# Kernel optimization log

Measured on AMD Instinct MI355X. Metric: run time of the kernel, lower is better.

## Reference

```python
import jax, jax.numpy as jnp
import numpy as np

NJ = 12
# shift buffer: inverse of the fixed 12x12 permutation matrix (= its transpose)
_idx = np.array([0, 1, 6, 2, 3, 8, 9, 7, 4, 5, 10, 11])
_P = np.zeros((NJ, NJ), np.float32)
_P[np.arange(NJ), _idx] = 1.0
SHIFT = jnp.asarray(_P.T)


def _bn(x, g, b, eps=1e-5):
    # BatchNorm2d in training mode: biased var over (batch, positions) per channel
    m = x.mean(axis=(0, 1), keepdims=True)
    v = x.var(axis=(0, 1), keepdims=True)
    return (x - m) * jax.lax.rsqrt(v + eps) * g + b


def setup_inputs() -> dict:
    key = jax.random.key(0)
    ks = jax.random.split(key, 10)
    B, D, E = 16384, 128, 128
    Din = D + E
    f32 = jnp.float32
    inp = {
        "gout": jax.random.normal(ks[0], (B, NJ, D), f32),
        "eout": jax.random.normal(ks[1], (B, NJ, E), f32),
        "ev_shift": jax.random.uniform(ks[2], (NJ, NJ), f32),
        "ve_shift": jax.random.uniform(ks[3], (NJ, NJ), f32),
        "W_ev": jax.random.normal(ks[4], (D, Din), f32) * 0.001,
        "W_ve": jax.random.normal(ks[5], (D, Din), f32) * 0.001,
        "W1": jax.random.normal(ks[6], (D, 3 * D), f32) * 0.001,
        "W2": jax.random.normal(ks[7], (D, 3 * D), f32) * 0.001,
        "W3": jax.random.normal(ks[8], (D, 2 * D), f32) * 0.001,
        "W4": jax.random.normal(ks[9], (D, 3 * D), f32) * 0.001,
    }
    for name in ["ev", "ve", "1", "2", "3", "4"]:
        inp["g_" + name] = jnp.ones((D,), f32)
        inp["b_" + name] = jnp.zeros((D,), f32)
    return inp


def reference(gout, eout, ev_shift, ve_shift, W_ev, g_ev, b_ev, W_ve, g_ve, b_ve,
              W1, g_1, b_1, W2, g_2, b_2, W3, g_3, b_3, W4, g_4, b_4):
    # gout: [B, 12, D], eout: [B, 12, E]
    ev_g = jnp.einsum('ij,bjd->bid', ev_shift, gout)
    ve_g = jnp.einsum('ij,bjd->bid', ve_shift, gout)
    # conv1x1 over channel dim == linear over feature dim; BN stats over (B, joints)
    ef = jax.nn.relu(_bn(jnp.einsum('bnc,dc->bnd', jnp.concatenate([eout, ev_g], -1), W_ev), g_ev, b_ev))
    vf = jax.nn.relu(_bn(jnp.einsum('bnc,dc->bnd', jnp.concatenate([ve_g, eout], -1), W_ve), g_ve, b_ve))
    # node_res blocks: per-group gather+concat -> linear -> BN (stats over B*group_positions)
    op1 = _bn(jnp.concatenate([ef[:, 0], ef[:, 1], ef[:, 5]], -1)[:, None] @ W1.T, g_1, b_1)
    op2_in = jnp.stack([
        jnp.concatenate([vf[:, 0], ef[:, 3], ef[:, 7]], -1),
        jnp.concatenate([vf[:, 5], ef[:, 7], ef[:, 8]], -1)], axis=1)
    op2 = _bn(op2_in @ W2.T, g_2, b_2)
    op3_in = jnp.stack([
        jnp.concatenate([vf[:, 1], ef[:, 2]], -1),
        jnp.concatenate([vf[:, 3], ef[:, 4]], -1),
        jnp.concatenate([vf[:, 8], ef[:, 9]], -1),
        jnp.concatenate([vf[:, 10], ef[:, 11]], -1)], axis=1)
    op3 = _bn(op3_in @ W3.T, g_3, b_3)
    op4 = _bn(jnp.concatenate([vf[:, 6], vf[:, 7], ef[:, 10]], -1)[:, None] @ W4.T, g_4, b_4)
    op5 = jnp.stack([vf[:, 2], vf[:, 4], vf[:, 9], vf[:, 11]], axis=1)
    res = jnp.concatenate([op1, op2, op3, op4, op5], axis=1)  # [B, 12, D]
    res = jnp.einsum('ij,bjd->bid', SHIFT, res)
    return jax.nn.relu(gout + res)
```

## Files before the change

### kernel.cpp

```cpp
#include <hip/hip_runtime.h>
#include <hip/hip_bf16.h>

#define BTOT 16384
typedef unsigned short u16;
typedef __attribute__((ext_vector_type(8))) short bf16x8;
typedef __attribute__((ext_vector_type(8))) unsigned short u16x8;
typedef __attribute__((ext_vector_type(4))) float f32x4;

#define MFMA16(a, b, c) __builtin_amdgcn_mfma_f32_16x16x32_bf16(a, b, c, 0, 0, 0)
#define NSLOT 16

__device__ __forceinline__ u16 f2b(float f) {
  unsigned int i = __float_as_uint(f);
  return (u16)((i + 0x7FFFu + ((i >> 16) & 1u)) >> 16);
}
__device__ __forceinline__ float b2f(u16 u) {
  return __uint_as_float(((unsigned int)u) << 16);
}
__device__ __forceinline__ unsigned pk2(float x, float y) {
  __hip_bfloat162 h = __float22bfloat162_rn(make_float2(x, y));
  unsigned r; __builtin_memcpy(&r, &h, 4); return r;
}
__device__ __forceinline__ bf16x8 pack8(float4 lo, float4 hi) {
  union { unsigned u[4]; bf16x8 v; } r;
  r.u[0] = pk2(lo.x, lo.y); r.u[1] = pk2(lo.z, lo.w);
  r.u[2] = pk2(hi.x, hi.y); r.u[3] = pk2(hi.z, hi.w);
  return r.v;
}
__device__ __forceinline__ void glds16(const void* g, void* l) {
  __builtin_amdgcn_global_load_lds(
      (const __attribute__((address_space(1))) void*)g,
      (__attribute__((address_space(3))) void*)l, 16, 0, 0);
}

__device__ const int c_mb[8][3]  = {{0,0,0},{1,0,0},{1,0,0},{1,0,0},{1,0,0},{1,0,0},{1,0,0},{1,1,0}};
__device__ const int c_mj[8][3]  = {{0,1,5},{0,3,7},{5,7,8},{1,2,0},{3,4,0},{8,9,0},{10,11,0},{6,7,10}};
__device__ const int c_opof[8]   = {0,1,1,2,2,2,2,3};
__device__ const int c_jmap[12]  = {0,1,3,4,8,9,2,7,5,6,10,11};
__device__ const int c_vj[4]     = {2,4,9,11};

__global__ __launch_bounds__(256) void k_prep(
    const float* __restrict__ wev, const float* __restrict__ wve,
    const float* __restrict__ w1, const float* __restrict__ w2,
    const float* __restrict__ w3, const float* __restrict__ w4,
    u16* __restrict__ wb, float* __restrict__ stats)
{
  int id = blockIdx.x * 256 + threadIdx.x;
  if (blockIdx.x == 0) {
    for (int i = threadIdx.x; i < NSLOT * 1536; i += 256) stats[i] = 0.f;
  }
  const float* src; int base, K, local;
  if (id < 32768)       { src = wev; base = 0;      K = 256; local = id; }
  else if (id < 65536)  { src = wve; base = 32768;  K = 256; local = id - 32768; }
  else if (id < 114688) { src = w1;  base = 65536;  K = 384; local = id - 65536; }
  else if (id < 163840) { src = w2;  base = 114688; K = 384; local = id - 114688; }
  else if (id < 196608) { src = w3;  base = 163840; K = 256; local = id - 163840; }
  else if (id < 245760) { src = w4;  base = 196608; K = 384; local = id - 245760 + 49152; }
  else return;
  if (id >= 196608 && id < 245760) local = id - 196608;
  int d = local / K, k = local - d * K;
  int dk = (base == 32768) ? (k ^ 128) : k;
  int dest = base + (dk >> 6) * 8192 + d * 64 + ((dk & 63) ^ ((d & 7) << 3));
  wb[dest] = f2b(src[local]);
}

__global__ __launch_bounds__(256, 2) void k_stage1(
    const float* __restrict__ gout, const float* __restrict__ eout,
    const float* __restrict__ evs, const float* __restrict__ ves,
    const u16* __restrict__ wb_ev, const u16* __restrict__ wb_ve,
    u16* __restrict__ y_ev, u16* __restrict__ y_ve, float* __restrict__ stats)
{
  __shared__ __align__(16) char lds[81920];
  char* se = lds;
  char* sm = lds + 24576;
  char* sw = lds + 49152;
  float* s_red = (float*)(lds + 49152);

  const int tid = threadIdx.x;
  const int l = tid & 63, wv = tid >> 6;
  const int wm = wv >> 1, wn = wv & 1;
  const int b0 = blockIdx.x * 8;
  const int kq = (l >> 4) * 8;
  const int bb = tid >> 5;
  const int d4 = (tid & 31) * 4;

  auto wstage = [&](const u16* wmat, int c, char* buf) {
    char* wvb = buf + wv * 1024;
    #pragma unroll
    for (int q = 0; q < 4; ++q)
      glds16(&wmat[c * 8192 + tid * 8 + q * 2048], wvb + q * 4096);
  };

  wstage(wb_ev, 0, sw);

  {
    float mev[12][4];
    #pragma unroll
    for (int n = 0; n < 12; ++n)
      #pragma unroll
      for (int q = 0; q < 4; ++q) mev[n][q] = 0.f;
    #pragma unroll
    for (int j = 0; j < 12; ++j) {
      float4 g4 = *(const float4*)&gout[((size_t)(b0 + bb) * 12 + j) * 128 + d4];
      float4 e4 = *(const float4*)&eout[((size_t)(b0 + bb) * 12 + j) * 128 + d4];
      int row = bb * 12 + j;
      uint2 ep = make_uint2(pk2(e4.x, e4.y), pk2(e4.z, e4.w));
      *(uint2*)(se + row * 256 + ((d4 * 2) ^ ((row & 7) << 4))) = ep;
      #pragma unroll
      for (int n = 0; n < 12; ++n) {
        float w = evs[n * 12 + j];
        mev[n][0] = fmaf(w, g4.x, mev[n][0]); mev[n][1] = fmaf(w, g4.y, mev[n][1]);
        mev[n][2] = fmaf(w, g4.z, mev[n][2]); mev[n][3] = fmaf(w, g4.w, mev[n][3]);
      }
    }
    #pragma unroll
    for (int n = 0; n < 12; ++n) {
      int row = bb * 12 + n;
      uint2 mp = make_uint2(pk2(mev[n][0], mev[n][1]), pk2(mev[n][2], mev[n][3]));
      *(uint2*)(sm + row * 256 + ((d4 * 2) ^ ((row & 7) << 4))) = mp;
    }
  }

  float sE[4] = {0,0,0,0}, qE[4] = {0,0,0,0}, sV[4] = {0,0,0,0}, qV[4] = {0,0,0,0};

  auto run_pass = [&](const u16* wmat, const u16* nextw, u16* yout, char* dump,
                      float* sS, float* qS) {
    f32x4 acc[3][4];
    #pragma unroll
    for (int mi = 0; mi < 3; ++mi)
      #pragma unroll
      for (int ni = 0; ni < 4; ++ni) acc[mi][ni] = (f32x4){0.f, 0.f, 0.f, 0.f};

    for (int c = 0; c < 4; ++c) {
      __syncthreads();
      if (c < 3) wstage(wmat, c + 1, sw + (((c + 1) & 1) ? 16384 : 0));
      else if (nextw) wstage(nextw, 0, sw);
      const char* xb = (c < 2) ? se : sm;
      const char* swb = sw + ((c & 1) ? 16384 : 0);
      #pragma unroll
      for (int kt = 0; kt < 2; ++kt) {
        bf16x8 a[3], bq[4];
        const int kb = (((c & 1) * 64 + kt * 32 + kq)) * 2;
        #pragma unroll
        for (int mi = 0; mi < 3; ++mi) {
          int row = (wm * 3 + mi) * 16 + (l & 15);
          a[mi] = *(const bf16x8*)(xb + row * 256 + (kb ^ ((row & 7) << 4)));
        }
        const int kw = (kt * 32 + kq) * 2;
        #pragma unroll
        for (int ni = 0; ni < 4; ++ni) {
          int n = (wn * 4 + ni) * 16 + (l & 15);
          bq[ni] = *(const bf16x8*)(swb + n * 128 + (kw ^ ((n & 7) << 4)));
        }
        #pragma unroll
        for (int mi = 0; mi < 3; ++mi)
          #pragma unroll
          for (int ni = 0; ni < 4; ++ni)
            acc[mi][ni] = MFMA16(a[mi], bq[ni], acc[mi][ni]);
      }
    }
    __syncthreads();
    #pragma unroll
    for (int mi = 0; mi < 3; ++mi)
      #pragma unroll
      for (int ni = 0; ni < 4; ++ni)
        #pragma unroll
        for (int q = 0; q < 4; ++q) {
          float v = acc[mi][ni][q];
          sS[ni] += v; qS[ni] += v * v;
          int row = (wm * 3 + mi) * 16 + (l >> 4) * 4 + q;
          int cb = ((wn * 4 + ni) * 16 + (l & 15)) * 2;
          *(u16*)(dump + row * 256 + (cb ^ ((row & 7) << 4))) = f2b(v);
        }
    __syncthreads();
    #pragma unroll
    for (int q = 0; q < 6; ++q) {
      int i = tid + q * 256;
      int row = i >> 4, cb = (i & 15) * 16;
      u16x8 v = *(const u16x8*)(dump + row * 256 + (cb ^ ((row & 7) << 4)));
      *(u16x8*)&yout[(size_t)(b0 * 12 + row) * 128 + (i & 15) * 8] = v;
    }
    __syncthreads();
  };

  run_pass(wb_ev, wb_ve, y_ev, sm, sE, qE);

  {
    float mve[12][4];
    #pragma unroll
    for (int n = 0; n < 12; ++n)
      #pragma unroll
      for (int q = 0; q < 4; ++q) mve[n][q] = 0.f;
    #pragma unroll
    for (int j = 0; j < 12; ++j) {
      float4 g4 = *(const float4*)&gout[((size_t)(b0 + bb) * 12 + j) * 128 + d4];
      #pragma unroll
      for (int n = 0; n < 12; ++n) {
        float w = ves[n * 12 + j];
        mve[n][0] = fmaf(w, g4.x, mve[n][0]); mve[n][1] = fmaf(w, g4.y, mve[n][1]);
        mve[n][2] = fmaf(w, g4.z, mve[n][2]); mve[n][3] = fmaf(w, g4.w, mve[n][3]);
      }
    }
    #pragma unroll
    for (int n = 0; n < 12; ++n) {
      int row = bb * 12 + n;
      uint2 mp = make_uint2(pk2(mve[n][0], mve[n][1]), pk2(mve[n][2], mve[n][3]));
      *(uint2*)(sm + row * 256 + ((d4 * 2) ^ ((row & 7) << 4))) = mp;
    }
  }

  run_pass(wb_ve, (const u16*)nullptr, y_ve, se, sV, qV);

  s_red[tid] = 0.f; s_red[tid + 256] = 0.f;
  __syncthreads();
  #pragma unroll
  for (int ni = 0; ni < 4; ++ni) {
    float a1 = sE[ni], b1 = qE[ni], a2 = sV[ni], b2 = qV[ni];
    a1 += __shfl_xor(a1, 16); a1 += __shfl_xor(a1, 32);
    b1 += __shfl_xor(b1, 16); b1 += __shfl_xor(b1, 32);
    a2 += __shfl_xor(a2, 16); a2 += __shfl_xor(a2, 32);
    b2 += __shfl_xor(b2, 16); b2 += __shfl_xor(b2, 32);
    if (l < 16) {
      int ch = (wn * 4 + ni) * 16 + l;
      atomicAdd(&s_red[ch], a1);       atomicAdd(&s_red[128 + ch], b1);
      atomicAdd(&s_red[256 + ch], a2); atomicAdd(&s_red[384 + ch], b2);
    }
  }
  __syncthreads();
  const int sb = (blockIdx.x & (NSLOT - 1)) * 1536;
  atomicAdd(&stats[sb + tid], s_red[tid]);
  atomicAdd(&stats[sb + 256 + tid], s_red[256 + tid]);
}

__global__ void k_fin1(const float* __restrict__ stats, float* __restrict__ scale,
                       const float* __restrict__ gev, const float* __restrict__ bev,
                       const float* __restrict__ gve, const float* __restrict__ bve)
{
  int t = threadIdx.x;
  int m = t >> 7, d = t & 127;
  float s = 0.f, q = 0.f;
  #pragma unroll
  for (int sl = 0; sl < NSLOT; ++sl) {
    s += stats[sl * 1536 + m * 256 + d];
    q += stats[sl * 1536 + m * 256 + 128 + d];
  }
  float cnt = (float)(BTOT * 12);
  float mean = s / cnt, var = q / cnt - mean * mean;
  float rs = rsqrtf(var + 1e-5f);
  float g = m ? gve[d] : gev[d];
  float b = m ? bve[d] : bev[d];
  float a = g * rs;
  scale[m * 256 + d] = a;
  scale[m * 256 + 128 + d] = b - mean * a;
}

__global__ __launch_bounds__(256, 4) void k_stage2(
    const u16* __restrict__ y_ev, const u16* __restrict__ y_ve,
    const float* __restrict__ scale,
    const u16* __restrict__ wb1, const u16* __restrict__ wb2,
    const u16* __restrict__ wb3, const u16* __restrict__ wb4,
    u16* __restrict__ y_op, float* __restrict__ stats)
{
  __shared__ __align__(16) u16 s_w[128 * 64];
  __shared__ __align__(16) u16 s_d[32 * 128];
  __shared__ float s_scale[512];
  __shared__ float s_red[256];
  char* sw = (char*)s_w; char* sd = (char*)s_d;

  const int tid = threadIdx.x, l = tid & 63, wv = tid >> 6;
  const int mw = wv & 1, nw = wv >> 1;
  const int r = blockIdx.x & 7;
  const int b0 = (blockIdx.x >> 3) * 32;
  const int Kr = (r >= 3 && r <= 6) ? 256 : 384;
  const u16* wr = (r == 0) ? wb1 : (r <= 2) ? wb2 : (r <= 6) ? wb3 : wb4;
  const int o = c_opof[r];
  const int j0 = c_mj[r][0], j1 = c_mj[r][1], j2 = c_mj[r][2];
  const int m0 = c_mb[r][0], m1 = c_mb[r][1], m2 = c_mb[r][2];

  for (int i = tid; i < 512; i += 256) s_scale[i] = scale[i];
  s_red[tid] = 0.f;

  f32x4 acc[4];
  #pragma unroll
  for (int ni = 0; ni < 4; ++ni) acc[ni] = (f32x4){0.f, 0.f, 0.f, 0.f};

  const int nch = Kr >> 6;
  const int kq = (l >> 4) * 8;
  const int batch = b0 + mw * 16 + (l & 15);

  for (int c = 0; c < nch; ++c) {
    {
      char* wvb = sw + wv * 1024;
      #pragma unroll
      for (int q = 0; q < 4; ++q)
        glds16(&wr[c * 8192 + tid * 8 + q * 2048], wvb + q * 4096);
    }
    __syncthreads();
    const int s = c >> 1;
    const int j = (s == 0) ? j0 : (s == 1) ? j1 : j2;
    const int mb = (s == 0) ? m0 : (s == 1) ? m1 : m2;
    const int sb = mb ? 256 : 0;
    const u16* ys = mb ? y_ve : y_ev;
    #pragma unroll
    for (int kt = 0; kt < 2; ++kt) {
      const int chan = (c & 1) * 64 + kt * 32 + kq;
      u16x8 u = *(const u16x8*)&ys[((size_t)batch * 12 + j) * 128 + chan];
      float4 a0 = *(const float4*)&s_scale[sb + chan];
      float4 a1 = *(const float4*)&s_scale[sb + chan + 4];
      float4 c0 = *(const float4*)&s_scale[sb + 128 + chan];
      float4 c1 = *(const float4*)&s_scale[sb + 128 + chan + 4];
      float4 lo, hi;
      lo.x = fmaxf(fmaf(b2f(u[0]), a0.x, c0.x), 0.f);
      lo.y = fmaxf(fmaf(b2f(u[1]), a0.y, c0.y), 0.f);
      lo.z = fmaxf(fmaf(b2f(u[2]), a0.z, c0.z), 0.f);
      lo.w = fmaxf(fmaf(b2f(u[3]), a0.w, c0.w), 0.f);
      hi.x = fmaxf(fmaf(b2f(u[4]), a1.x, c1.x), 0.f);
      hi.y = fmaxf(fmaf(b2f(u[5]), a1.y, c1.y), 0.f);
      hi.z = fmaxf(fmaf(b2f(u[6]), a1.z, c1.z), 0.f);
      hi.w = fmaxf(fmaf(b2f(u[7]), a1.w, c1.w), 0.f);
      bf16x8 afrag = pack8(lo, hi);
      const int kw = (kt * 32 + kq) * 2;
      #pragma unroll
      for (int ni = 0; ni < 4; ++ni) {
        int n = (nw * 4 + ni) * 16 + (l & 15);
        bf16x8 b = *(const bf16x8*)(sw + n * 128 + (kw ^ ((n & 7) << 4)));
        acc[ni] = MFMA16(afrag, b, acc[ni]);
      }
    }
    __syncthreads();
  }

  #pragma unroll
  for (int ni = 0; ni < 4; ++ni) {
    float s1 = 0.f, q1 = 0.f;
    #pragma unroll
    for (int q = 0; q < 4; ++q) {
      float v = acc[ni][q];
      s1 += v; q1 += v * v;
      int row = mw * 16 + (l >> 4) * 4 + q;
      int cb = ((nw * 4 + ni) * 16 + (l & 15)) * 2;
      *(u16*)(sd + row * 256 + (cb ^ ((row & 7) << 4))) = f2b(v);
    }
    s1 += __shfl_xor(s1, 16); s1 += __shfl_xor(s1, 32);
    q1 += __shfl_xor(q1, 16); q1 += __shfl_xor(q1, 32);
    if (l < 16) {
      int ch = (nw * 4 + ni) * 16 + l;
      atomicAdd(&s_red[ch], s1);
      atomicAdd(&s_red[128 + ch], q1);
    }
  }
  __syncthreads();
  #pragma unroll
  for (int q = 0; q < 2; ++q) {
    int i = tid + q * 256;
    int row = i >> 4, cb = (i & 15) * 16;
    u16x8 v = *(const u16x8*)(sd + row * 256 + (cb ^ ((row & 7) << 4)));
    *(u16x8*)&y_op[((size_t)(b0 + row) * 8 + r) * 128 + (i & 15) * 8] = v;
  }
  const int sb2 = (blockIdx.x & (NSLOT - 1)) * 1536;
  atomicAdd(&stats[sb2 + 512 + o * 256 + tid], s_red[tid]);
}

__global__ void k_fin2(const float* __restrict__ stats, float* __restrict__ scale,
    const float* __restrict__ g1, const float* __restrict__ b1,
    const float* __restrict__ g2, const float* __restrict__ b2,
    const float* __restrict__ g3, const float* __restrict__ b3,
    const float* __restrict__ g4, const float* __restrict__ b4)
{
  int t = threadIdx.x;
  int o = t >> 7, d = t & 127;
  float s = 0.f, q = 0.f;
  #pragma unroll
  for (int sl = 0; sl < NSLOT; ++sl) {
    s += stats[sl * 1536 + 512 + o * 256 + d];
    q += stats[sl * 1536 + 512 + o * 256 + 128 + d];
  }
  float cnt = (o == 0 || o == 3) ? 16384.f : (o == 1 ? 32768.f : 65536.f);
  float mean = s / cnt, var = q / cnt - mean * mean;
  float rs = rsqrtf(var + 1e-5f);
  const float* gp = (o == 0) ? g1 : (o == 1) ? g2 : (o == 2) ? g3 : g4;
  const float* bp = (o == 0) ? b1 : (o == 1) ? b2 : (o == 2) ? b3 : b4;
  float a = gp[d] * rs;
  scale[512 + o * 256 + d] = a;
  scale[512 + o * 256 + 128 + d] = bp[d] - mean * a;
}

__global__ __launch_bounds__(256) void k_stage3(
    const u16* __restrict__ y_op, const u16* __restrict__ y_ve,
    const float* __restrict__ scale, const float* __restrict__ gout,
    float* __restrict__ out)
{
  const int stride = gridDim.x * 256;
  const int total = BTOT * 12 * 32;
  for (int id = blockIdx.x * 256 + threadIdx.x; id < total; id += stride) {
    int b = id / 384;
    int rem = id - b * 384;
    int i = rem >> 5;
    int d4 = (rem & 31) * 4;
    int j = c_jmap[i];
    float4 v;
    if (j < 8) {
      ushort4 u = *(const ushort4*)&y_op[((size_t)b * 8 + j) * 128 + d4];
      int o = c_opof[j];
      float4 a4 = *(const float4*)&scale[512 + o * 256 + d4];
      float4 c4 = *(const float4*)&scale[512 + o * 256 + 128 + d4];
      v.x = fmaf(b2f(u.x), a4.x, c4.x);
      v.y = fmaf(b2f(u.y), a4.y, c4.y);
      v.z = fmaf(b2f(u.z), a4.z, c4.z);
      v.w = fmaf(b2f(u.w), a4.w, c4.w);
    } else {
      int jv = c_vj[j - 8];
      ushort4 u = *(const ushort4*)&y_ve[((size_t)b * 12 + jv) * 128 + d4];
      float4 a4 = *(const float4*)&scale[256 + d4];
      float4 c4 = *(const float4*)&scale[384 + d4];
      v.x = fmaxf(fmaf(b2f(u.x), a4.x, c4.x), 0.f);
      v.y = fmaxf(fmaf(b2f(u.y), a4.y, c4.y), 0.f);
      v.z = fmaxf(fmaf(b2f(u.z), a4.z, c4.z), 0.f);
      v.w = fmaxf(fmaf(b2f(u.w), a4.w, c4.w), 0.f);
    }
    float4 g4 = *(const float4*)&gout[((size_t)b * 12 + i) * 128 + d4];
    float4 r4;
    r4.x = fmaxf(g4.x + v.x, 0.f);
    r4.y = fmaxf(g4.y + v.y, 0.f);
    r4.z = fmaxf(g4.z + v.z, 0.f);
    r4.w = fmaxf(g4.w + v.w, 0.f);
    *(float4*)&out[((size_t)b * 12 + i) * 128 + d4] = r4;
  }
}

extern "C" void kernel_launch(void* const* d_in, const int* in_sizes, int n_in,
                              void* d_out, int out_size, void* d_ws, size_t ws_size,
                              hipStream_t stream) {
  (void)in_sizes; (void)n_in; (void)out_size; (void)ws_size;
  const float* gout = (const float*)d_in[0];
  const float* eout = (const float*)d_in[1];
  const float* evs  = (const float*)d_in[2];
  const float* ves  = (const float*)d_in[3];
  const float* wev  = (const float*)d_in[4];
  const float* wve  = (const float*)d_in[5];
  const float* w1   = (const float*)d_in[6];
  const float* w2   = (const float*)d_in[7];
  const float* w3   = (const float*)d_in[8];
  const float* w4   = (const float*)d_in[9];
  const float* g_ev = (const float*)d_in[10]; const float* b_ev = (const float*)d_in[11];
  const float* g_ve = (const float*)d_in[12]; const float* b_ve = (const float*)d_in[13];
  const float* g_1  = (const float*)d_in[14]; const float* b_1  = (const float*)d_in[15];
  const float* g_2  = (const float*)d_in[16]; const float* b_2  = (const float*)d_in[17];
  const float* g_3  = (const float*)d_in[18]; const float* b_3  = (const float*)d_in[19];
  const float* g_4  = (const float*)d_in[20]; const float* b_4  = (const float*)d_in[21];

  char* ws = (char*)d_ws;
  u16*   y_ev  = (u16*)ws;
  u16*   y_ve  = (u16*)(ws + 50331648);
  u16*   y_op  = (u16*)(ws + 100663296);
  u16*   wb    = (u16*)(ws + 134217728);
  float* stats = (float*)(ws + 134709248);
  float* scale = (float*)(ws + 134807552);

  k_prep<<<960, 256, 0, stream>>>(wev, wve, w1, w2, w3, w4, wb, stats);
  k_stage1<<<2048, 256, 0, stream>>>(gout, eout, evs, ves, wb, wb + 32768, y_ev, y_ve, stats);
  k_fin1<<<1, 256, 0, stream>>>(stats, scale, g_ev, b_ev, g_ve, b_ve);
  k_stage2<<<4096, 256, 0, stream>>>(y_ev, y_ve, scale, wb + 65536, wb + 114688, wb + 163840, wb + 196608, y_op, stats);
  k_fin2<<<1, 512, 0, stream>>>(stats, scale, g_1, b_1, g_2, b_2, g_3, b_3, g_4, b_4);
  k_stage3<<<4096, 256, 0, stream>>>(y_op, y_ve, scale, gout, (float*)d_out);
}
```

Measured before the change: 207.8 us.

## Hold eout MFMA fragments in registers and halve weight staging to raise occupancy

Stage 1 no longer stages eout through LDS. Each wave loads its eout A-fragments straight from global into registers and packs them to bf16. The weight staging buffer is split into half-chunks of 32 K-columns with a new 64-byte-row swizzle, and the prep kernel lays out the ev/ve weights to match. Shared memory drops from 80 KB to about 42 KB and launch bounds rise to 3 blocks per CU, aiming for more occupancy. In exchange there are more barriers per pass and more registers held for eout fragments, which could cause spills under the tighter register budget.

Result: slower. 308.8 us (+48.6%).

```diff
diff --git a/kernel.cpp b/kernel.cpp
--- a/kernel.cpp
+++ b/kernel.cpp
@@ -55,26 +55,27 @@
   else if (id < 114688) { src = w1;  base = 65536;  K = 384; local = id - 65536; }
   else if (id < 163840) { src = w2;  base = 114688; K = 384; local = id - 114688; }
   else if (id < 196608) { src = w3;  base = 163840; K = 256; local = id - 163840; }
-  else if (id < 245760) { src = w4;  base = 196608; K = 384; local = id - 245760 + 49152; }
+  else if (id < 245760) { src = w4;  base = 196608; K = 384; local = id - 196608; }
   else return;
-  if (id >= 196608 && id < 245760) local = id - 196608;
   int d = local / K, k = local - d * K;
-  int dk = (base == 32768) ? (k ^ 128) : k;
-  int dest = base + (dk >> 6) * 8192 + d * 64 + ((dk & 63) ^ ((d & 7) << 3));
-  wb[dest] = f2b(src[local]);
-}
-
-__global__ __launch_bounds__(256, 2) void k_stage1(
+  if (base < 65536) {
+    int dk = (base == 32768) ? (k ^ 128) : k;
+    int c = dk >> 6, kt = (dk >> 5) & 1, kk = dk & 31;
+    wb[base + c * 8192 + kt * 4096 + d * 32 + (kk ^ ((d & 3) << 3))] = f2b(src[local]);
+  } else {
+    wb[base + (k >> 6) * 8192 + d * 64 + ((k & 63) ^ ((d & 7) << 3))] = f2b(src[local]);
+  }
+}
+
+__global__ __launch_bounds__(256, 3) void k_stage1(
     const float* __restrict__ gout, const float* __restrict__ eout,
     const float* __restrict__ evs, const float* __restrict__ ves,
     const u16* __restrict__ wb_ev, const u16* __restrict__ wb_ve,
     u16* __restrict__ y_ev, u16* __restrict__ y_ve, float* __restrict__ stats)
 {
-  __shared__ __align__(16) char lds[81920];
-  char* se = lds;
-  char* sm = lds + 24576;
-  char* sw = lds + 49152;
-  float* s_red = (float*)(lds + 49152);
+  __shared__ __align__(16) char sm[24576];
+  __shared__ __align__(16) char sw[16384];
+  __shared__ float s_red[512];
 
   const int tid = threadIdx.x;
   const int l = tid & 63, wv = tid >> 6;
@@ -84,11 +85,12 @@
   const int bb = tid >> 5;
   const int d4 = (tid & 31) * 4;
 
-  auto wstage = [&](const u16* wmat, int c, char* buf) {
+  auto wstage = [&](const u16* wmat, int p, char* buf) {
+    const u16* pb = wmat + (p >> 1) * 8192 + (p & 1) * 4096;
     char* wvb = buf + wv * 1024;
     #pragma unroll
-    for (int q = 0; q < 4; ++q)
-      glds16(&wmat[c * 8192 + tid * 8 + q * 2048], wvb + q * 4096);
+    for (int q = 0; q < 2; ++q)
+      glds16(&pb[tid * 8 + q * 2048], wvb + q * 4096);
   };
 
   wstage(wb_ev, 0, sw);
@@ -102,10 +104,6 @@
     #pragma unroll
     for (int j = 0; j < 12; ++j) {
       float4 g4 = *(const float4*)&gout[((size_t)(b0 + bb) * 12 + j) * 128 + d4];
-      float4 e4 = *(const float4*)&eout[((size_t)(b0 + bb) * 12 + j) * 128 + d4];
-      int row = bb * 12 + j;
-      uint2 ep = make_uint2(pk2(e4.x, e4.y), pk2(e4.z, e4.w));
-      *(uint2*)(se + row * 256 + ((d4 * 2) ^ ((row & 7) << 4))) = ep;
       #pragma unroll
       for (int n = 0; n < 12; ++n) {
         float w = evs[n * 12 + j];
@@ -121,9 +119,23 @@
     }
   }
 
+  bf16x8 ea[2][2][3];
+  #pragma unroll
+  for (int c2 = 0; c2 < 2; ++c2)
+    #pragma unroll
+    for (int kt = 0; kt < 2; ++kt)
+      #pragma unroll
+      for (int mi = 0; mi < 3; ++mi) {
+        int row = wm * 48 + mi * 16 + (l & 15);
+        const float* p = eout + ((size_t)(b0 * 12) + row) * 128 + c2 * 64 + kt * 32 + kq;
+        float4 u0 = *(const float4*)p;
+        float4 u1 = *(const float4*)(p + 4);
+        ea[c2][kt][mi] = pack8(u0, u1);
+      }
+
   float sE[4] = {0,0,0,0}, qE[4] = {0,0,0,0}, sV[4] = {0,0,0,0}, qV[4] = {0,0,0,0};
 
-  auto run_pass = [&](const u16* wmat, const u16* nextw, u16* yout, char* dump,
+  auto run_pass = [&](const u16* wmat, const u16* nextw, u16* yout,
                       float* sS, float* qS) {
     f32x4 acc[3][4];
     #pragma unroll
@@ -131,33 +143,35 @@
       #pragma unroll
       for (int ni = 0; ni < 4; ++ni) acc[mi][ni] = (f32x4){0.f, 0.f, 0.f, 0.f};
 
-    for (int c = 0; c < 4; ++c) {
+    #pragma unroll
+    for (int p = 0; p < 8; ++p) {
       __syncthreads();
-      if (c < 3) wstage(wmat, c + 1, sw + (((c + 1) & 1) ? 16384 : 0));
+      if (p < 7) wstage(wmat, p + 1, sw + (((p + 1) & 1) ? 8192 : 0));
       else if (nextw) wstage(nextw, 0, sw);
-      const char* xb = (c < 2) ? se : sm;
-      const char* swb = sw + ((c & 1) ? 16384 : 0);
-      #pragma unroll
-      for (int kt = 0; kt < 2; ++kt) {
-        bf16x8 a[3], bq[4];
+      const int c = p >> 1, kt = p & 1;
+      bf16x8 a[3], bq[4];
+      if (c < 2) {
+        #pragma unroll
+        for (int mi = 0; mi < 3; ++mi) a[mi] = ea[c][kt][mi];
+      } else {
         const int kb = (((c & 1) * 64 + kt * 32 + kq)) * 2;
         #pragma unroll
         for (int mi = 0; mi < 3; ++mi) {
-          int row = (wm * 3 + mi) * 16 + (l & 15);
-          a[mi] = *(const bf16x8*)(xb + row * 256 + (kb ^ ((row & 7) << 4)));
+          int row = wm * 48 + mi * 16 + (l & 15);
+          a[mi] = *(const bf16x8*)(sm + row * 256 + (kb ^ ((row & 7) << 4)));
         }
-        const int kw = (kt * 32 + kq) * 2;
+      }
+      const char* swb = sw + ((p & 1) ? 8192 : 0);
+      #pragma unroll
+      for (int ni = 0; ni < 4; ++ni) {
+        int n = (wn * 4 + ni) * 16 + (l & 15);
+        bq[ni] = *(const bf16x8*)(swb + n * 64 + (((l >> 4) * 16) ^ ((n & 3) << 4)));
+      }
+      #pragma unroll
+      for (int mi = 0; mi < 3; ++mi)
         #pragma unroll
-        for (int ni = 0; ni < 4; ++ni) {
-          int n = (wn * 4 + ni) * 16 + (l & 15);
-          bq[ni] = *(const bf16x8*)(swb + n * 128 + (kw ^ ((n & 7) << 4)));
-        }
-        #pragma unroll
-        for (int mi = 0; mi < 3; ++mi)
-          #pragma unroll
-          for (int ni = 0; ni < 4; ++ni)
-            acc[mi][ni] = MFMA16(a[mi], bq[ni], acc[mi][ni]);
-      }
+        for (int ni = 0; ni < 4; ++ni)
+          acc[mi][ni] = MFMA16(a[mi], bq[ni], acc[mi][ni]);
     }
     __syncthreads();
     #pragma unroll
@@ -168,22 +182,22 @@
         for (int q = 0; q < 4; ++q) {
           float v = acc[mi][ni][q];
           sS[ni] += v; qS[ni] += v * v;
-          int row = (wm * 3 + mi) * 16 + (l >> 4) * 4 + q;
+          int row = wm * 48 + mi * 16 + (l >> 4) * 4 + q;
           int cb = ((wn * 4 + ni) * 16 + (l & 15)) * 2;
-          *(u16*)(dump + row * 256 + (cb ^ ((row & 7) << 4))) = f2b(v);
+          *(u16*)(sm + row * 256 + (cb ^ ((row & 7) << 4))) = f2b(v);
         }
     __syncthreads();
     #pragma unroll
     for (int q = 0; q < 6; ++q) {
       int i = tid + q * 256;
       int row = i >> 4, cb = (i & 15) * 16;
-      u16x8 v = *(const u16x8*)(dump + row * 256 + (cb ^ ((row & 7) << 4)));
+      u16x8 v = *(const u16x8*)(sm + row * 256 + (cb ^ ((row & 7) << 4)));
       *(u16x8*)&yout[(size_t)(b0 * 12 + row) * 128 + (i & 15) * 8] = v;
     }
     __syncthreads();
   };
 
-  run_pass(wb_ev, wb_ve, y_ev, sm, sE, qE);
+  run_pass(wb_ev, wb_ve, y_ev, sE, qE);
 
   {
     float mve[12][4];
@@ -209,7 +223,7 @@
     }
   }
 
-  run_pass(wb_ve, (const u16*)nullptr, y_ve, se, sV, qV);
+  run_pass(wb_ve, (const u16*)nullptr, y_ve, sV, qV);
 
   s_red[tid] = 0.f; s_red[tid + 256] = 0.f;
   __syncthreads();
```
